# Kernel tuning notes

Measured on AMD Instinct MI355X. Metric: run time of the kernel, lower is better.

Reference implementation:

```python
import jax, jax.numpy as jnp
import numpy as np

B, IN_CHAN, L = 16, 16, 4096
OUTC, KS = 64, 7

def _conv1d(x, w, b, stride=1, pad=0):
    # x: (N, Cin, L), w: (Cout, Cin, K)
    y = jax.lax.conv_general_dilated(x, w, (stride,), [(pad, pad)],
                                     dimension_numbers=('NCH', 'OIH', 'NCH'))
    return y + b[None, :, None]

def setup_inputs() -> dict:
    key = jax.random.key(0)
    ks = jax.random.split(key, 7)
    x = jax.random.normal(ks[0], (B, 1, L, IN_CHAN), dtype=jnp.float32)
    # offset-predicting conv (inc=1 -> KS offsets), k=3 pad=1
    p_w = jax.random.normal(ks[1], (KS, 1, 3), dtype=jnp.float32) * 0.1
    p_b = jax.random.normal(ks[2], (KS,), dtype=jnp.float32) * 0.1
    # modulation conv (inc=1 -> KS masks), k=3 pad=1
    m_w = jax.random.normal(ks[3], (KS, 1, 3), dtype=jnp.float32) * 0.1
    m_b = jax.random.normal(ks[4], (KS,), dtype=jnp.float32) * 0.1
    # main conv over resampled signal: (1 -> OUTC), k=KS, stride=KS
    c_w = jax.random.normal(ks[5], (OUTC, 1, KS), dtype=jnp.float32) * (1.0 / np.sqrt(KS))
    c_b = jax.random.normal(ks[6], (OUTC,), dtype=jnp.float32) * 0.1
    return {"x": x, "p_w": p_w, "p_b": p_b, "m_w": m_w, "m_b": m_b,
            "c_w": c_w, "c_b": c_b}

def _deform_conv1d(xs, p_w, p_b, m_w, m_b, c_w, c_b):
    # xs: (N, 1, L) single-channel 1D signal; returns (N, OUTC, L)
    N, _, Lx = xs.shape
    ksz = c_w.shape[2]
    offset = _conv1d(xs, p_w, p_b, pad=1)              # (N, ks, L)
    m = jax.nn.sigmoid(_conv1d(xs, m_w, m_b, pad=1))   # (N, ks, L)
    p_n = jnp.arange(-(ksz - 1) // 2, (ksz - 1) // 2 + 1, dtype=xs.dtype)  # kernel offsets
    p_0 = jnp.arange(1, Lx + 1, dtype=xs.dtype)        # base grid (starts at 1, as in deform-conv-v2)
    p = p_0[None, None, :] + p_n[None, :, None] + offset  # (N, ks, L)
    p = jnp.transpose(p, (0, 2, 1))                       # (N, L, ks)
    q_lt = jnp.clip(jnp.floor(jax.lax.stop_gradient(p)), 0, Lx - 1)
    q_rb = jnp.clip(q_lt + 1, 0, Lx - 1)
    p = jnp.clip(p, 0, Lx - 1)
    g_lt = 1 + (q_lt - p)                               # linear-interp weights
    g_rb = 1 - (q_rb - p)
    sig = xs[:, 0, :]                                   # (N, L) since inc == 1
    idx_lt = q_lt.astype(jnp.int32).reshape(N, Lx * ksz)
    idx_rb = q_rb.astype(jnp.int32).reshape(N, Lx * ksz)
    x_lt = jnp.take_along_axis(sig, idx_lt, axis=1).reshape(N, Lx, ksz)
    x_rb = jnp.take_along_axis(sig, idx_rb, axis=1).reshape(N, Lx, ksz)
    x_off = (g_lt * x_lt + g_rb * x_rb) * jnp.transpose(m, (0, 2, 1))  # (N, L, ks)
    x_off = x_off.reshape(N, 1, Lx * ksz)
    return _conv1d(x_off, c_w, c_b, stride=ksz)         # (N, OUTC, L)

def reference(x, p_w, p_b, m_w, m_b, c_w, c_b):
    # x: (B, 1, L, C); same DeformConv1D applied independently to every last-dim slice.
    # Fold the slice loop into the batch dim (same math, no Python loop).
    Bx, _, Lx, Cx = x.shape
    xs = jnp.transpose(x, (0, 3, 1, 2)).reshape(Bx * Cx, 1, Lx)
    y = _deform_conv1d(xs, p_w, p_b, m_w, m_b, c_w, c_b)  # (B*C, OUTC, L)
    y = y.reshape(Bx, Cx, -1, Lx)
    return jnp.transpose(y, (0, 2, 3, 1))                 # (B, OUTC, L, C)
```

## Files before the change

### kernel.cpp

```cpp
#include <hip/hip_runtime.h>
#include <math.h>

#define BB   16
#define CC   16
#define LL   4096
#define OUTC 64
#define KS   7

typedef float vfloat2 __attribute__((ext_vector_type(2)));
typedef float vfloat4 __attribute__((ext_vector_type(4)));

__global__ __launch_bounds__(256) void transpose_kernel(
    const float* __restrict__ x, float* __restrict__ xT)
{
    __shared__ float tile[64 * 17];
    const int b   = blockIdx.x >> 6;
    const int l0  = (blockIdx.x & 63) * 64;
    const int tid = threadIdx.x;
    {
        const int lo = tid >> 2, cq = (tid & 3) * 4;
        float4 v = *(const float4*)(x + ((size_t)(b * LL + l0 + lo)) * CC + cq);
        tile[lo * 17 + cq + 0] = v.x;
        tile[lo * 17 + cq + 1] = v.y;
        tile[lo * 17 + cq + 2] = v.z;
        tile[lo * 17 + cq + 3] = v.w;
    }
    __syncthreads();
    {
        const int c = tid >> 4, li = (tid & 15) * 4;
        float4 v;
        v.x = tile[(li + 0) * 17 + c];
        v.y = tile[(li + 1) * 17 + c];
        v.z = tile[(li + 2) * 17 + c];
        v.w = tile[(li + 3) * 17 + c];
        *(float4*)(xT + ((size_t)(b * CC + c)) * LL + l0 + li) = v;
    }
}

template <bool USE_XT>
__global__ __launch_bounds__(256, 6) void deform_conv_kernel(
    const float* __restrict__ x,
    const float* __restrict__ xT,
    const float* __restrict__ p_w, const float* __restrict__ p_b,
    const float* __restrict__ m_w, const float* __restrict__ m_b,
    const float* __restrict__ c_w, const float* __restrict__ c_b,
    float* __restrict__ out)
{
    __shared__ float cw_lds[OUTC * 8];
    __shared__ float pw_lds[KS * 4];
    __shared__ float mw_lds[KS * 4];

    const int tid = threadIdx.x;

    for (int i = tid; i < OUTC * 8; i += 256) {
        int o = i >> 3, j = i & 7;
        cw_lds[i] = (j < 7) ? c_w[o * 7 + j] : c_b[o];
    }
    if (tid < KS * 4) {
        int k = tid >> 2, j = tid & 3;
        pw_lds[tid] = (j < 3) ? p_w[k * 3 + j] : p_b[k];
        mw_lds[tid] = (j < 3) ? m_w[k * 3 + j] : m_b[k];
    }
    __syncthreads();

    const int b     = blockIdx.x >> 7;
    const int ltile = blockIdx.x & 127;
    const int l     = ltile * 32 + (tid >> 3);
    const int c0    = (tid & 7) * 2;

    const float* xb = x + (size_t)b * (LL * CC);

    float s_m1[2] = {0.f, 0.f};
    float s_p1[2] = {0.f, 0.f};
    float s_0[2];
    {
        float2 v0 = *(const float2*)(xb + l * CC + c0);
        s_0[0] = v0.x; s_0[1] = v0.y;
        if (l > 0) {
            float2 vm = *(const float2*)(xb + (l - 1) * CC + c0);
            s_m1[0] = vm.x; s_m1[1] = vm.y;
        }
        if (l < LL - 1) {
            float2 vp = *(const float2*)(xb + (l + 1) * CC + c0);
            s_p1[0] = vp.x; s_p1[1] = vp.y;
        }
    }

    float xoff[2][KS];
    const float pl = (float)(l + 1);
    const float* xt0 = USE_XT ? (xT + (size_t)(b * CC + c0) * LL) : nullptr;
    #pragma unroll
    for (int k = 0; k < KS; ++k) {
        float4 pw = *(const float4*)(pw_lds + k * 4);
        float4 mw = *(const float4*)(mw_lds + k * 4);
        const float pn = (float)(k - 3);
        #pragma unroll
        for (int c = 0; c < 2; ++c) {
            float off  = pw.w + pw.x * s_m1[c] + pw.y * s_0[c] + pw.z * s_p1[c];
            float mact = mw.w + mw.x * s_m1[c] + mw.y * s_0[c] + mw.z * s_p1[c];
            float mm   = 1.f / (1.f + __expf(-mact));

            float p    = pl + pn + off;
            float qltf = fminf(fmaxf(floorf(p), 0.f), (float)(LL - 1));
            float qrbf = fminf(qltf + 1.f, (float)(LL - 1));
            float pc   = fminf(fmaxf(p, 0.f), (float)(LL - 1));
            float glt  = 1.f + (qltf - pc);
            float grb  = 1.f - (qrbf - pc);

            float xlt, xrb;
            if (USE_XT) {
                int iload = (int)fminf(qltf, (float)(LL - 2));
                const float* pr = xt0 + (size_t)c * LL + iload;
                float va = pr[0];
                float vb = pr[1];
                xlt = (qltf >= (float)(LL - 1)) ? vb : va;
                xrb = vb;
            } else {
                int ilt = (int)qltf;
                int irb = (int)qrbf;
                xlt = xb[ilt * CC + c0 + c];
                xrb = xb[irb * CC + c0 + c];
            }
            xoff[c][k] = (glt * xlt + grb * xrb) * mm;
        }
    }

    float* outp = out + ((size_t)(b * OUTC) * LL + l) * CC + c0;
    #pragma unroll 4
    for (int o = 0; o < OUTC; ++o) {
        float4 w0 = *(const float4*)(cw_lds + o * 8);
        float4 w1 = *(const float4*)(cw_lds + o * 8 + 4);
        vfloat2 res;
        #pragma unroll
        for (int c = 0; c < 2; ++c) {
            float a = w1.w;
            a += w0.x * xoff[c][0];
            a += w0.y * xoff[c][1];
            a += w0.z * xoff[c][2];
            a += w0.w * xoff[c][3];
            a += w1.x * xoff[c][4];
            a += w1.y * xoff[c][5];
            a += w1.z * xoff[c][6];
            res[c] = a;
        }
        __builtin_nontemporal_store(res, (vfloat2*)(outp + (size_t)o * (LL * CC)));
    }
}

extern "C" void kernel_launch(void* const* d_in, const int* in_sizes, int n_in,
                              void* d_out, int out_size, void* d_ws, size_t ws_size,
                              hipStream_t stream) {
    const float* x   = (const float*)d_in[0];
    const float* p_w = (const float*)d_in[1];
    const float* p_b = (const float*)d_in[2];
    const float* m_w = (const float*)d_in[3];
    const float* m_b = (const float*)d_in[4];
    const float* c_w = (const float*)d_in[5];
    const float* c_b = (const float*)d_in[6];
    float* out = (float*)d_out;

    const size_t xt_bytes = (size_t)BB * CC * LL * sizeof(float);
    if (d_ws != nullptr && ws_size >= xt_bytes) {
        float* xT = (float*)d_ws;
        transpose_kernel<<<dim3(BB * 64), dim3(256), 0, stream>>>(x, xT);
        deform_conv_kernel<true><<<dim3(BB * 128), dim3(256), 0, stream>>>(
            x, xT, p_w, p_b, m_w, m_b, c_w, c_b, out);
    } else {
        deform_conv_kernel<false><<<dim3(BB * 128), dim3(256), 0, stream>>>(
            x, nullptr, p_w, p_b, m_w, m_b, c_w, c_b, out);
    }
}
```

Baseline: 300.0 us.

## Process four channels per thread, drop LDS weight staging, use float4 stores

Each thread now handles four channels instead of two, so blocks shrink to 128 threads and the input loads and output stores widen to float4. The shared-memory staging of the conv weights and its __syncthreads are removed; weights are read directly from global memory as uniform (likely scalar) loads. The nontemporal stores are replaced by ordinary vector stores. This trades fewer threads and more registers per thread for wider memory transactions and no LDS or barrier overhead.

```diff
diff --git a/kernel.cpp b/kernel.cpp
--- a/kernel.cpp
+++ b/kernel.cpp
@@ -7,7 +7,6 @@
 #define OUTC 64
 #define KS   7
 
-typedef float vfloat2 __attribute__((ext_vector_type(2)));
 typedef float vfloat4 __attribute__((ext_vector_type(4)));
 
 __global__ __launch_bounds__(256) void transpose_kernel(
@@ -38,7 +37,7 @@
 }
 
 template <bool USE_XT>
-__global__ __launch_bounds__(256, 6) void deform_conv_kernel(
+__global__ __launch_bounds__(128, 6) void deform_conv_kernel(
     const float* __restrict__ x,
     const float* __restrict__ xT,
     const float* __restrict__ p_w, const float* __restrict__ p_b,
@@ -46,58 +45,44 @@
     const float* __restrict__ c_w, const float* __restrict__ c_b,
     float* __restrict__ out)
 {
-    __shared__ float cw_lds[OUTC * 8];
-    __shared__ float pw_lds[KS * 4];
-    __shared__ float mw_lds[KS * 4];
-
-    const int tid = threadIdx.x;
-
-    for (int i = tid; i < OUTC * 8; i += 256) {
-        int o = i >> 3, j = i & 7;
-        cw_lds[i] = (j < 7) ? c_w[o * 7 + j] : c_b[o];
-    }
-    if (tid < KS * 4) {
-        int k = tid >> 2, j = tid & 3;
-        pw_lds[tid] = (j < 3) ? p_w[k * 3 + j] : p_b[k];
-        mw_lds[tid] = (j < 3) ? m_w[k * 3 + j] : m_b[k];
-    }
-    __syncthreads();
-
+    const int tid   = threadIdx.x;
     const int b     = blockIdx.x >> 7;
     const int ltile = blockIdx.x & 127;
-    const int l     = ltile * 32 + (tid >> 3);
-    const int c0    = (tid & 7) * 2;
+    const int l     = ltile * 32 + (tid >> 2);
+    const int c0    = (tid & 3) * 4;
 
     const float* xb = x + (size_t)b * (LL * CC);
 
-    float s_m1[2] = {0.f, 0.f};
-    float s_p1[2] = {0.f, 0.f};
-    float s_0[2];
+    float s_m1[4] = {0.f, 0.f, 0.f, 0.f};
+    float s_p1[4] = {0.f, 0.f, 0.f, 0.f};
+    float s_0[4];
     {
-        float2 v0 = *(const float2*)(xb + l * CC + c0);
-        s_0[0] = v0.x; s_0[1] = v0.y;
+        float4 v0 = *(const float4*)(xb + l * CC + c0);
+        s_0[0] = v0.x; s_0[1] = v0.y; s_0[2] = v0.z; s_0[3] = v0.w;
         if (l > 0) {
-            float2 vm = *(const float2*)(xb + (l - 1) * CC + c0);
-            s_m1[0] = vm.x; s_m1[1] = vm.y;
+            float4 vm = *(const float4*)(xb + (l - 1) * CC + c0);
+            s_m1[0] = vm.x; s_m1[1] = vm.y; s_m1[2] = vm.z; s_m1[3] = vm.w;
         }
         if (l < LL - 1) {
-            float2 vp = *(const float2*)(xb + (l + 1) * CC + c0);
-            s_p1[0] = vp.x; s_p1[1] = vp.y;
+            float4 vp = *(const float4*)(xb + (l + 1) * CC + c0);
+            s_p1[0] = vp.x; s_p1[1] = vp.y; s_p1[2] = vp.z; s_p1[3] = vp.w;
         }
     }
 
-    float xoff[2][KS];
+    float xoff[4][KS];
     const float pl = (float)(l + 1);
     const float* xt0 = USE_XT ? (xT + (size_t)(b * CC + c0) * LL) : nullptr;
     #pragma unroll
     for (int k = 0; k < KS; ++k) {
-        float4 pw = *(const float4*)(pw_lds + k * 4);
-        float4 mw = *(const float4*)(mw_lds + k * 4);
+        const float pw0 = p_w[k * 3 + 0], pw1 = p_w[k * 3 + 1],
+                    pw2 = p_w[k * 3 + 2], pbk = p_b[k];
+        const float mw0 = m_w[k * 3 + 0], mw1 = m_w[k * 3 + 1],
+                    mw2 = m_w[k * 3 + 2], mbk = m_b[k];
         const float pn = (float)(k - 3);
         #pragma unroll
-        for (int c = 0; c < 2; ++c) {
-            float off  = pw.w + pw.x * s_m1[c] + pw.y * s_0[c] + pw.z * s_p1[c];
-            float mact = mw.w + mw.x * s_m1[c] + mw.y * s_0[c] + mw.z * s_p1[c];
+        for (int c = 0; c < 4; ++c) {
+            float off  = pbk + pw0 * s_m1[c] + pw1 * s_0[c] + pw2 * s_p1[c];
+            float mact = mbk + mw0 * s_m1[c] + mw1 * s_0[c] + mw2 * s_p1[c];
             float mm   = 1.f / (1.f + __expf(-mact));
 
             float p    = pl + pn + off;
@@ -128,22 +113,24 @@
     float* outp = out + ((size_t)(b * OUTC) * LL + l) * CC + c0;
     #pragma unroll 4
     for (int o = 0; o < OUTC; ++o) {
-        float4 w0 = *(const float4*)(cw_lds + o * 8);
-        float4 w1 = *(const float4*)(cw_lds + o * 8 + 4);
-        vfloat2 res;
+        const float* cw = c_w + o * 7;
+        const float w0 = cw[0], w1 = cw[1], w2 = cw[2], w3 = cw[3],
+                    w4 = cw[4], w5 = cw[5], w6 = cw[6];
+        const float bias = c_b[o];
+        vfloat4 res;
         #pragma unroll
-        for (int c = 0; c < 2; ++c) {
-            float a = w1.w;
-            a += w0.x * xoff[c][0];
-            a += w0.y * xoff[c][1];
-            a += w0.z * xoff[c][2];
-            a += w0.w * xoff[c][3];
-            a += w1.x * xoff[c][4];
-            a += w1.y * xoff[c][5];
-            a += w1.z * xoff[c][6];
+        for (int c = 0; c < 4; ++c) {
+            float a = bias;
+            a += w0 * xoff[c][0];
+            a += w1 * xoff[c][1];
+            a += w2 * xoff[c][2];
+            a += w3 * xoff[c][3];
+            a += w4 * xoff[c][4];
+            a += w5 * xoff[c][5];
+            a += w6 * xoff[c][6];
             res[c] = a;
         }
-        __builtin_nontemporal_store(res, (vfloat2*)(outp + (size_t)o * (LL * CC)));
+        *(vfloat4*)(outp + (size_t)o * (LL * CC)) = res;
     }
 }
 
@@ -163,10 +150,10 @@
     if (d_ws != nullptr && ws_size >= xt_bytes) {
         float* xT = (float*)d_ws;
         transpose_kernel<<<dim3(BB * 64), dim3(256), 0, stream>>>(x, xT);
-        deform_conv_kernel<true><<<dim3(BB * 128), dim3(256), 0, stream>>>(
+        deform_conv_kernel<true><<<dim3(BB * 128), dim3(128), 0, stream>>>(
             x, xT, p_w, p_b, m_w, m_b, c_w, c_b, out);
     } else {
-        deform_conv_kernel<false><<<dim3(BB * 128), dim3(256), 0, stream>>>(
+        deform_conv_kernel<false><<<dim3(BB * 128), dim3(128), 0, stream>>>(
             x, nullptr, p_w, p_b, m_w, m_b, c_w, c_b, out);
     }
 }
```

New measurement: 294.8 us. About the same (-1.7%).
